# Kernel optimization log

Measured on AMD Instinct MI355X. Metric: run time of the kernel, lower is better.

Reference implementation:

```python
import jax, jax.numpy as jnp
import numpy as np

V, E, H, A, S, B = 32000, 1024, 1024, 10, 512, 64


def setup_inputs() -> dict:
    key = jax.random.key(0)
    ks = jax.random.split(key, 12)
    s = 0.02
    return {
        "dec_input": jax.random.randint(ks[0], (B, 1), 0, V, dtype=jnp.int32),
        "dec_hidden": jax.random.normal(ks[1], (1, B, H), jnp.float32),
        "enc_outputs": jax.random.normal(ks[2], (S, B, H), jnp.float32),
        "emb": jax.random.normal(ks[3], (V, E), jnp.float32) * s,
        "Wa1": jax.random.normal(ks[4], (A, 2 * H), jnp.float32) * s,  # attention layer 1, no bias
        "Wa2": jax.random.normal(ks[5], (1, A), jnp.float32) * s,      # attention layer 2, no bias
        "W_ih": jax.random.normal(ks[6], (3 * H, E + H), jnp.float32) * s,  # GRU input weights (r,z,n)
        "W_hh": jax.random.normal(ks[7], (3 * H, H), jnp.float32) * s,      # GRU hidden weights (r,z,n)
        "b_ih": jnp.zeros((3 * H,), jnp.float32),
        "b_hh": jnp.zeros((3 * H,), jnp.float32),
        "W_out": jax.random.normal(ks[8], (V, H), jnp.float32) * s,
        "b_out": jnp.zeros((V,), jnp.float32),
    }


def reference(dec_input, dec_hidden, enc_outputs, emb, Wa1, Wa2, W_ih, W_hh, b_ih, b_hh, W_out, b_out):
    h_last = dec_hidden[-1]  # [B, H]
    # Bahdanau additive attention over encoder time steps (axis 0)
    hh = jnp.broadcast_to(h_last[None], enc_outputs.shape)        # [S, B, H]
    feats = jnp.concatenate([hh, enc_outputs], axis=-1)           # [S, B, 2H]
    e = jnp.tanh(feats @ Wa1.T) @ Wa2.T                           # [S, B, 1]
    alpha = jax.nn.softmax(e, axis=0)                             # softmax over seq
    c = jnp.sum(alpha * enc_outputs, axis=0)                      # [B, H]
    # embedding lookup for the single decoder step
    x = emb[dec_input[:, 0]]                                      # [B, E]
    xc = jnp.concatenate([x, c], axis=1)                          # [B, E+H]
    # single-step GRU (PyTorch gate order: r, z, n)
    gi = xc @ W_ih.T + b_ih                                       # [B, 3H]
    gh = h_last @ W_hh.T + b_hh                                   # [B, 3H]
    i_r, i_z, i_n = jnp.split(gi, 3, axis=1)
    h_r, h_z, h_n = jnp.split(gh, 3, axis=1)
    r = jax.nn.sigmoid(i_r + h_r)
    z = jax.nn.sigmoid(i_z + h_z)
    n = jnp.tanh(i_n + r * h_n)
    h_new = (1.0 - z) * n + z * h_last                            # [B, H]
    logits = h_new @ W_out.T + b_out                              # [B, V]
    return logits, h_new[None]                                    # ([B,V], [1,B,H])
```

## Files before the change

kernel.cpp:

```cpp
#include <hip/hip_runtime.h>
#include <math.h>

#define Vv 32000
#define Ee 1024
#define Hh 1024
#define Aa 10
#define Ss 512
#define Bb 64
#define Mm (Ss * Bb)

typedef __attribute__((ext_vector_type(8))) short bf16x8;
typedef __attribute__((ext_vector_type(4))) short s16x4;
typedef __attribute__((ext_vector_type(4))) float f32x4;

__device__ inline short f2bf(float f) {
    union { float f; unsigned int u; } v;
    v.f = f;
    unsigned int r = (v.u + 0x7FFFu + ((v.u >> 16) & 1u)) >> 16;
    return (short)r;
}

__device__ inline bf16x8 cvt8(float4 lo, float4 hi) {
    bf16x8 r;
    r[0] = f2bf(lo.x); r[1] = f2bf(lo.y); r[2] = f2bf(lo.z); r[3] = f2bf(lo.w);
    r[4] = f2bf(hi.x); r[5] = f2bf(hi.y); r[6] = f2bf(hi.z); r[7] = f2bf(hi.w);
    return r;
}

__global__ __launch_bounds__(256) void hpart_kernel(const float* __restrict__ Wa1,
                                                    const float* __restrict__ h,
                                                    float* __restrict__ hpart) {
    __shared__ float part[4][16];
    const int b = blockIdx.x, t = threadIdx.x;
    const int w = t >> 6, lane = t & 63;
    const float* hb_ = h + (size_t)b * Hh;
    float p[Aa];
#pragma unroll
    for (int a = 0; a < Aa; a++) p[a] = 0.f;
#pragma unroll
    for (int i = 0; i < 4; i++) {
        const int k = w * 256 + i * 64 + lane;
        const float hv = hb_[k];
#pragma unroll
        for (int a = 0; a < Aa; a++) p[a] += Wa1[a * (2 * Hh) + k] * hv;
    }
#pragma unroll
    for (int a = 0; a < Aa; a++) {
        float v = p[a];
        v += __shfl_xor(v, 1, 64);
        v += __shfl_xor(v, 2, 64);
        v += __shfl_xor(v, 4, 64);
        v += __shfl_xor(v, 8, 64);
        v += __shfl_xor(v, 16, 64);
        v += __shfl_xor(v, 32, 64);
        if (lane == 0) part[w][a] = v;
    }
    __syncthreads();
    if (t < Aa)
        hpart[b * 16 + t] = part[0][t] + part[1][t] + part[2][t] + part[3][t];
}

__global__ __launch_bounds__(256) void scores_e_kernel(
    const float* __restrict__ enc,
    const float* __restrict__ Wa1,
    const float* __restrict__ Wa2,
    const float* __restrict__ hpart,
    float* __restrict__ e_t) {
    const int t = threadIdx.x;
    const int w = t >> 6, lane = t & 63;
    const int col = lane & 15, quad = lane >> 4;
    const int m0 = (blockIdx.x * 4 + w) * 16;
    const int bb = m0 & 63;
    const bool valid = (col < Aa);
    const int wa_row = valid ? col : 0;

    const float* erow = enc + (size_t)(m0 + col) * Hh + quad * 8;
    const float* wrow = Wa1 + (size_t)wa_row * (2 * Hh) + Hh + quad * 8;

    f32x4 acc = {0.f, 0.f, 0.f, 0.f};
#pragma unroll 4
    for (int c = 0; c < 32; c++) {
        float4 a0 = *(const float4*)(erow + c * 32);
        float4 a1 = *(const float4*)(erow + c * 32 + 4);
        bf16x8 af = cvt8(a0, a1);
        bf16x8 bf;
        if (valid) {
            float4 b0 = *(const float4*)(wrow + c * 32);
            float4 b1 = *(const float4*)(wrow + c * 32 + 4);
            bf = cvt8(b0, b1);
        } else {
            bf = (bf16x8){0, 0, 0, 0, 0, 0, 0, 0};
        }
        acc = __builtin_amdgcn_mfma_f32_16x16x32_bf16(af, bf, acc, 0, 0, 0);
    }

    const float w2 = valid ? Wa2[col] : 0.f;
    float v[4];
#pragma unroll
    for (int r = 0; r < 4; r++) {
        const int mr = quad * 4 + r;
        const float hp = valid ? hpart[(bb + mr) * 16 + col] : 0.f;
        v[r] = w2 * tanhf(acc[r] + hp);
    }
#pragma unroll
    for (int r = 0; r < 4; r++) {
        v[r] += __shfl_xor(v[r], 1, 16);
        v[r] += __shfl_xor(v[r], 2, 16);
        v[r] += __shfl_xor(v[r], 4, 16);
        v[r] += __shfl_xor(v[r], 8, 16);
    }
    if (col == 0) {
#pragma unroll
        for (int r = 0; r < 4; r++) {
            const int m = m0 + quad * 4 + r;
            e_t[(size_t)(m & 63) * Ss + (m >> 6)] = v[r];
        }
    }
}

__global__ __launch_bounds__(256) void context_kernel(const float* __restrict__ enc,
                                                      const float* __restrict__ e_t,
                                                      float* __restrict__ cpart) {
    __shared__ float al[Ss];
    __shared__ float sred[8];
    const int b = blockIdx.x, sc = blockIdx.y, t = threadIdx.x;
    const int w = t >> 6, lane = t & 63;

    const float x0 = e_t[(size_t)b * Ss + t];
    const float x1 = e_t[(size_t)b * Ss + 256 + t];
    float mx = fmaxf(x0, x1);
    mx = fmaxf(mx, __shfl_xor(mx, 1, 64));
    mx = fmaxf(mx, __shfl_xor(mx, 2, 64));
    mx = fmaxf(mx, __shfl_xor(mx, 4, 64));
    mx = fmaxf(mx, __shfl_xor(mx, 8, 64));
    mx = fmaxf(mx, __shfl_xor(mx, 16, 64));
    mx = fmaxf(mx, __shfl_xor(mx, 32, 64));
    if (lane == 0) sred[w] = mx;
    __syncthreads();
    const float MX = fmaxf(fmaxf(sred[0], sred[1]), fmaxf(sred[2], sred[3]));
    const float e0 = expf(x0 - MX), e1 = expf(x1 - MX);
    al[t] = e0;
    al[t + 256] = e1;
    float su = e0 + e1;
    su += __shfl_xor(su, 1, 64);
    su += __shfl_xor(su, 2, 64);
    su += __shfl_xor(su, 4, 64);
    su += __shfl_xor(su, 8, 64);
    su += __shfl_xor(su, 16, 64);
    su += __shfl_xor(su, 32, 64);
    if (lane == 0) sred[4 + w] = su;
    __syncthreads();
    const float inv = 1.f / (sred[4] + sred[5] + sred[6] + sred[7]);

    const float4* enc4 = (const float4*)enc;
    float4 acc = {0.f, 0.f, 0.f, 0.f};
    const int s0 = sc * 32;
#pragma unroll 4
    for (int i = 0; i < 32; ++i) {
        const int s = s0 + i;
        const float a = al[s] * inv;
        float4 ev = enc4[(size_t)(s * Bb + b) * 256 + t];
        acc.x += a * ev.x;
        acc.y += a * ev.y;
        acc.z += a * ev.z;
        acc.w += a * ev.w;
    }
    ((float4*)cpart)[((size_t)sc * Bb + b) * 256 + t] = acc;
}

__global__ __launch_bounds__(256) void xc_kernel(const int* __restrict__ dec_input,
                                                 const float* __restrict__ emb,
                                                 const float* __restrict__ cpart,
                                                 const float* __restrict__ h,
                                                 short* __restrict__ xcb,
                                                 short* __restrict__ hb) {
    const int b = blockIdx.x, t = threadIdx.x;
    const int tok = dec_input[b];
    float4 cv = {0.f, 0.f, 0.f, 0.f};
#pragma unroll
    for (int p = 0; p < 16; p++) {
        float4 v = ((const float4*)cpart)[((size_t)p * Bb + b) * 256 + t];
        cv.x += v.x; cv.y += v.y; cv.z += v.z; cv.w += v.w;
    }
    float4 ev = ((const float4*)(emb + (size_t)tok * Ee))[t];
    float4 hv = ((const float4*)(h + (size_t)b * Hh))[t];
    s16x4 e4 = {f2bf(ev.x), f2bf(ev.y), f2bf(ev.z), f2bf(ev.w)};
    s16x4 c4 = {f2bf(cv.x), f2bf(cv.y), f2bf(cv.z), f2bf(cv.w)};
    s16x4 h4v = {f2bf(hv.x), f2bf(hv.y), f2bf(hv.z), f2bf(hv.w)};
    ((s16x4*)(xcb + (size_t)b * 2048))[t] = e4;
    ((s16x4*)(xcb + (size_t)b * 2048 + 1024))[t] = c4;
    ((s16x4*)(hb + (size_t)b * 1024))[t] = h4v;
}

template<int K, int KLEN>
__global__ __launch_bounds__(256) void gemm_mfma_kernel(
    const short* __restrict__ Abf,
    const float* __restrict__ W,
    const float* __restrict__ bias,
    float* __restrict__ C,
    int N) {
    const int t = threadIdx.x;
    const int w = t >> 6, lane = t & 63;
    const int col = lane & 15, quad = lane >> 4;
    const int n0 = blockIdx.x * 64 + w * 16;
    const int kb0 = blockIdx.y * KLEN;

    f32x4 acc[4];
#pragma unroll
    for (int mt = 0; mt < 4; mt++) acc[mt] = (f32x4){0.f, 0.f, 0.f, 0.f};

    const float* wrow = W + (size_t)(n0 + col) * K + kb0 + quad * 8;
    const short* arow = Abf + (size_t)col * K + kb0 + quad * 8;

#pragma unroll 2
    for (int kb = 0; kb < KLEN; kb += 64) {
        float4 w0 = *(const float4*)(wrow + kb);
        float4 w1 = *(const float4*)(wrow + kb + 4);
        float4 w2 = *(const float4*)(wrow + kb + 32);
        float4 w3 = *(const float4*)(wrow + kb + 36);
        bf16x8 bf0 = cvt8(w0, w1);
        bf16x8 bf1 = cvt8(w2, w3);
        bf16x8 a0[4], a1[4];
#pragma unroll
        for (int mt = 0; mt < 4; mt++) {
            a0[mt] = *(const bf16x8*)(arow + (size_t)mt * 16 * K + kb);
            a1[mt] = *(const bf16x8*)(arow + (size_t)mt * 16 * K + kb + 32);
        }
#pragma unroll
        for (int mt = 0; mt < 4; mt++)
            acc[mt] = __builtin_amdgcn_mfma_f32_16x16x32_bf16(a0[mt], bf0, acc[mt], 0, 0, 0);
#pragma unroll
        for (int mt = 0; mt < 4; mt++)
            acc[mt] = __builtin_amdgcn_mfma_f32_16x16x32_bf16(a1[mt], bf1, acc[mt], 0, 0, 0);
    }

    const float bv = (bias != nullptr) ? bias[n0 + col] : 0.f;
    float* Cp = C + (size_t)blockIdx.y * 64 * N;
#pragma unroll
    for (int mt = 0; mt < 4; mt++) {
#pragma unroll
        for (int r = 0; r < 4; r++) {
            int m = mt * 16 + quad * 4 + r;
            Cp[(size_t)m * N + n0 + col] = acc[mt][r] + bv;
        }
    }
}

__global__ __launch_bounds__(256) void gru_kernel(const float* __restrict__ gip,
                                                  const float* __restrict__ ghp,
                                                  const float* __restrict__ b_ih,
                                                  const float* __restrict__ b_hh,
                                                  const float* __restrict__ h,
                                                  float* __restrict__ h_new,
                                                  short* __restrict__ hnb) {
    const int idx = blockIdx.x * 256 + threadIdx.x;
    const int b = idx >> 10, j = idx & 1023;
    const size_t base = (size_t)b * (3 * Hh);
    float ir = b_ih[j], iz = b_ih[Hh + j], in_ = b_ih[2 * Hh + j];
    float hr = b_hh[j], hz = b_hh[Hh + j], hn = b_hh[2 * Hh + j];
#pragma unroll
    for (int p = 0; p < 8; p++) {
        const float* g = gip + (size_t)p * Bb * 3 * Hh + base;
        ir += g[j]; iz += g[Hh + j]; in_ += g[2 * Hh + j];
    }
#pragma unroll
    for (int p = 0; p < 8; p++) {
        const float* g = ghp + (size_t)p * Bb * 3 * Hh + base;
        hr += g[j]; hz += g[Hh + j]; hn += g[2 * Hh + j];
    }
    float r = 1.f / (1.f + expf(-(ir + hr)));
    float z = 1.f / (1.f + expf(-(iz + hz)));
    float n = tanhf(in_ + r * hn);
    float val = (1.f - z) * n + z * h[idx];
    h_new[idx] = val;
    hnb[idx] = f2bf(val);
}

extern "C" void kernel_launch(void* const* d_in, const int* in_sizes, int n_in,
                              void* d_out, int out_size, void* d_ws, size_t ws_size,
                              hipStream_t stream) {
    const int* dec_input = (const int*)d_in[0];
    const float* dec_hidden = (const float*)d_in[1];
    const float* enc = (const float*)d_in[2];
    const float* emb = (const float*)d_in[3];
    const float* Wa1 = (const float*)d_in[4];
    const float* Wa2 = (const float*)d_in[5];
    const float* W_ih = (const float*)d_in[6];
    const float* W_hh = (const float*)d_in[7];
    const float* b_ih = (const float*)d_in[8];
    const float* b_hh = (const float*)d_in[9];
    const float* W_out = (const float*)d_in[10];
    const float* b_out = (const float*)d_in[11];

    float* out = (float*)d_out;
    float* logits = out;
    float* h_new = out + (size_t)Bb * Vv;

    float* ws = (float*)d_ws;
    float* hpart_ptr = ws;
    float* e_ptr = ws + 1024;
    short* xcb_ptr = (short*)(ws + 33792);
    short* hb_ptr = (short*)(ws + 99328);
    short* hnb_ptr = (short*)(ws + 132096);
    float* region1 = ws + 164864;
    float* region2 = ws + 1737728;
    float* cpart_ptr = region1;
    float* gip_ptr = region1;
    float* ghp_ptr = region2;

    hpart_kernel<<<Bb, 256, 0, stream>>>(Wa1, dec_hidden, hpart_ptr);
    scores_e_kernel<<<Mm / 64, 256, 0, stream>>>(enc, Wa1, Wa2, hpart_ptr, e_ptr);
    context_kernel<<<dim3(Bb, 16), 256, 0, stream>>>(enc, e_ptr, cpart_ptr);
    xc_kernel<<<Bb, 256, 0, stream>>>(dec_input, emb, cpart_ptr, dec_hidden,
                                      xcb_ptr, hb_ptr);

    gemm_mfma_kernel<2048, 256><<<dim3(3 * Hh / 64, 8), 256, 0, stream>>>(
        xcb_ptr, W_ih, nullptr, gip_ptr, 3 * Hh);
    gemm_mfma_kernel<1024, 128><<<dim3(3 * Hh / 64, 8), 256, 0, stream>>>(
        hb_ptr, W_hh, nullptr, ghp_ptr, 3 * Hh);

    gru_kernel<<<(Bb * Hh) / 256, 256, 0, stream>>>(gip_ptr, ghp_ptr, b_ih, b_hh,
                                                    dec_hidden, h_new, hnb_ptr);

    gemm_mfma_kernel<1024, 1024><<<dim3(Vv / 64, 1), 256, 0, stream>>>(
        hnb_ptr, W_out, b_out, logits, Vv);
}
```

Before: 447.2 us.

## Fuse all decoder stages into one cooperative persistent kernel with grid syncs

Replaces eight separate kernel launches with a single cooperative kernel of 512 blocks that runs each stage (hpart, scores, softmax-context, xc packing, GRU gemms, GRU cell, output projection) as a phase separated by grid-wide barriers. It also changes the work splits: the context reduction uses 8 sequence chunks instead of 16, and the W_hh gemm uses 2 K-splits instead of 8. The aim is to remove per-launch overhead and inter-kernel gaps. In exchange, phases such as the 500-block output gemm are limited to a fixed grid with 2 blocks per CU, and grid.sync costs are added.

```diff
diff --git a/kernel.cpp b/kernel.cpp
--- a/kernel.cpp
+++ b/kernel.cpp
@@ -1,5 +1,8 @@
 #include <hip/hip_runtime.h>
+#include <hip/hip_cooperative_groups.h>
 #include <math.h>
+
+namespace cg = cooperative_groups;
 
 #define Vv 32000
 #define Ee 1024
@@ -9,6 +12,8 @@
 #define Bb 64
 #define Mm (Ss * Bb)
 
+#define NBLK 512
+
 typedef __attribute__((ext_vector_type(8))) short bf16x8;
 typedef __attribute__((ext_vector_type(4))) short s16x4;
 typedef __attribute__((ext_vector_type(4))) float f32x4;
@@ -27,183 +32,15 @@
     return r;
 }
 
-__global__ __launch_bounds__(256) void hpart_kernel(const float* __restrict__ Wa1,
-                                                    const float* __restrict__ h,
-                                                    float* __restrict__ hpart) {
-    __shared__ float part[4][16];
-    const int b = blockIdx.x, t = threadIdx.x;
-    const int w = t >> 6, lane = t & 63;
-    const float* hb_ = h + (size_t)b * Hh;
-    float p[Aa];
-#pragma unroll
-    for (int a = 0; a < Aa; a++) p[a] = 0.f;
-#pragma unroll
-    for (int i = 0; i < 4; i++) {
-        const int k = w * 256 + i * 64 + lane;
-        const float hv = hb_[k];
-#pragma unroll
-        for (int a = 0; a < Aa; a++) p[a] += Wa1[a * (2 * Hh) + k] * hv;
-    }
-#pragma unroll
-    for (int a = 0; a < Aa; a++) {
-        float v = p[a];
-        v += __shfl_xor(v, 1, 64);
-        v += __shfl_xor(v, 2, 64);
-        v += __shfl_xor(v, 4, 64);
-        v += __shfl_xor(v, 8, 64);
-        v += __shfl_xor(v, 16, 64);
-        v += __shfl_xor(v, 32, 64);
-        if (lane == 0) part[w][a] = v;
-    }
-    __syncthreads();
-    if (t < Aa)
-        hpart[b * 16 + t] = part[0][t] + part[1][t] + part[2][t] + part[3][t];
-}
-
-__global__ __launch_bounds__(256) void scores_e_kernel(
-    const float* __restrict__ enc,
-    const float* __restrict__ Wa1,
-    const float* __restrict__ Wa2,
-    const float* __restrict__ hpart,
-    float* __restrict__ e_t) {
-    const int t = threadIdx.x;
-    const int w = t >> 6, lane = t & 63;
+template<int K, int KLEN>
+__device__ __forceinline__ void gemm_phase(const short* __restrict__ Abf,
+                                           const float* __restrict__ W,
+                                           const float* __restrict__ bias,
+                                           float* __restrict__ C, int N,
+                                           int nb, int kp, int w, int lane) {
     const int col = lane & 15, quad = lane >> 4;
-    const int m0 = (blockIdx.x * 4 + w) * 16;
-    const int bb = m0 & 63;
-    const bool valid = (col < Aa);
-    const int wa_row = valid ? col : 0;
-
-    const float* erow = enc + (size_t)(m0 + col) * Hh + quad * 8;
-    const float* wrow = Wa1 + (size_t)wa_row * (2 * Hh) + Hh + quad * 8;
-
-    f32x4 acc = {0.f, 0.f, 0.f, 0.f};
-#pragma unroll 4
-    for (int c = 0; c < 32; c++) {
-        float4 a0 = *(const float4*)(erow + c * 32);
-        float4 a1 = *(const float4*)(erow + c * 32 + 4);
-        bf16x8 af = cvt8(a0, a1);
-        bf16x8 bf;
-        if (valid) {
-            float4 b0 = *(const float4*)(wrow + c * 32);
-            float4 b1 = *(const float4*)(wrow + c * 32 + 4);
-            bf = cvt8(b0, b1);
-        } else {
-            bf = (bf16x8){0, 0, 0, 0, 0, 0, 0, 0};
-        }
-        acc = __builtin_amdgcn_mfma_f32_16x16x32_bf16(af, bf, acc, 0, 0, 0);
-    }
-
-    const float w2 = valid ? Wa2[col] : 0.f;
-    float v[4];
-#pragma unroll
-    for (int r = 0; r < 4; r++) {
-        const int mr = quad * 4 + r;
-        const float hp = valid ? hpart[(bb + mr) * 16 + col] : 0.f;
-        v[r] = w2 * tanhf(acc[r] + hp);
-    }
-#pragma unroll
-    for (int r = 0; r < 4; r++) {
-        v[r] += __shfl_xor(v[r], 1, 16);
-        v[r] += __shfl_xor(v[r], 2, 16);
-        v[r] += __shfl_xor(v[r], 4, 16);
-        v[r] += __shfl_xor(v[r], 8, 16);
-    }
-    if (col == 0) {
-#pragma unroll
-        for (int r = 0; r < 4; r++) {
-            const int m = m0 + quad * 4 + r;
-            e_t[(size_t)(m & 63) * Ss + (m >> 6)] = v[r];
-        }
-    }
-}
-
-__global__ __launch_bounds__(256) void context_kernel(const float* __restrict__ enc,
-                                                      const float* __restrict__ e_t,
-                                                      float* __restrict__ cpart) {
-    __shared__ float al[Ss];
-    __shared__ float sred[8];
-    const int b = blockIdx.x, sc = blockIdx.y, t = threadIdx.x;
-    const int w = t >> 6, lane = t & 63;
-
-    const float x0 = e_t[(size_t)b * Ss + t];
-    const float x1 = e_t[(size_t)b * Ss + 256 + t];
-    float mx = fmaxf(x0, x1);
-    mx = fmaxf(mx, __shfl_xor(mx, 1, 64));
-    mx = fmaxf(mx, __shfl_xor(mx, 2, 64));
-    mx = fmaxf(mx, __shfl_xor(mx, 4, 64));
-    mx = fmaxf(mx, __shfl_xor(mx, 8, 64));
-    mx = fmaxf(mx, __shfl_xor(mx, 16, 64));
-    mx = fmaxf(mx, __shfl_xor(mx, 32, 64));
-    if (lane == 0) sred[w] = mx;
-    __syncthreads();
-    const float MX = fmaxf(fmaxf(sred[0], sred[1]), fmaxf(sred[2], sred[3]));
-    const float e0 = expf(x0 - MX), e1 = expf(x1 - MX);
-    al[t] = e0;
-    al[t + 256] = e1;
-    float su = e0 + e1;
-    su += __shfl_xor(su, 1, 64);
-    su += __shfl_xor(su, 2, 64);
-    su += __shfl_xor(su, 4, 64);
-    su += __shfl_xor(su, 8, 64);
-    su += __shfl_xor(su, 16, 64);
-    su += __shfl_xor(su, 32, 64);
-    if (lane == 0) sred[4 + w] = su;
-    __syncthreads();
-    const float inv = 1.f / (sred[4] + sred[5] + sred[6] + sred[7]);
-
-    const float4* enc4 = (const float4*)enc;
-    float4 acc = {0.f, 0.f, 0.f, 0.f};
-    const int s0 = sc * 32;
-#pragma unroll 4
-    for (int i = 0; i < 32; ++i) {
-        const int s = s0 + i;
-        const float a = al[s] * inv;
-        float4 ev = enc4[(size_t)(s * Bb + b) * 256 + t];
-        acc.x += a * ev.x;
-        acc.y += a * ev.y;
-        acc.z += a * ev.z;
-        acc.w += a * ev.w;
-    }
-    ((float4*)cpart)[((size_t)sc * Bb + b) * 256 + t] = acc;
-}
-
-__global__ __launch_bounds__(256) void xc_kernel(const int* __restrict__ dec_input,
-                                                 const float* __restrict__ emb,
-                                                 const float* __restrict__ cpart,
-                                                 const float* __restrict__ h,
-                                                 short* __restrict__ xcb,
-                                                 short* __restrict__ hb) {
-    const int b = blockIdx.x, t = threadIdx.x;
-    const int tok = dec_input[b];
-    float4 cv = {0.f, 0.f, 0.f, 0.f};
-#pragma unroll
-    for (int p = 0; p < 16; p++) {
-        float4 v = ((const float4*)cpart)[((size_t)p * Bb + b) * 256 + t];
-        cv.x += v.x; cv.y += v.y; cv.z += v.z; cv.w += v.w;
-    }
-    float4 ev = ((const float4*)(emb + (size_t)tok * Ee))[t];
-    float4 hv = ((const float4*)(h + (size_t)b * Hh))[t];
-    s16x4 e4 = {f2bf(ev.x), f2bf(ev.y), f2bf(ev.z), f2bf(ev.w)};
-    s16x4 c4 = {f2bf(cv.x), f2bf(cv.y), f2bf(cv.z), f2bf(cv.w)};
-    s16x4 h4v = {f2bf(hv.x), f2bf(hv.y), f2bf(hv.z), f2bf(hv.w)};
-    ((s16x4*)(xcb + (size_t)b * 2048))[t] = e4;
-    ((s16x4*)(xcb + (size_t)b * 2048 + 1024))[t] = c4;
-    ((s16x4*)(hb + (size_t)b * 1024))[t] = h4v;
-}
-
-template<int K, int KLEN>
-__global__ __launch_bounds__(256) void gemm_mfma_kernel(
-    const short* __restrict__ Abf,
-    const float* __restrict__ W,
-    const float* __restrict__ bias,
-    float* __restrict__ C,
-    int N) {
-    const int t = threadIdx.x;
-    const int w = t >> 6, lane = t & 63;
-    const int col = lane & 15, quad = lane >> 4;
-    const int n0 = blockIdx.x * 64 + w * 16;
-    const int kb0 = blockIdx.y * KLEN;
+    const int n0 = nb * 64 + w * 16;
+    const int kb0 = kp * KLEN;
 
     f32x4 acc[4];
 #pragma unroll
@@ -235,7 +72,7 @@
     }
 
     const float bv = (bias != nullptr) ? bias[n0 + col] : 0.f;
-    float* Cp = C + (size_t)blockIdx.y * 64 * N;
+    float* Cp = C + (size_t)kp * 64 * N;
 #pragma unroll
     for (int mt = 0; mt < 4; mt++) {
 #pragma unroll
@@ -246,34 +83,223 @@
     }
 }
 
-__global__ __launch_bounds__(256) void gru_kernel(const float* __restrict__ gip,
-                                                  const float* __restrict__ ghp,
-                                                  const float* __restrict__ b_ih,
-                                                  const float* __restrict__ b_hh,
-                                                  const float* __restrict__ h,
-                                                  float* __restrict__ h_new,
-                                                  short* __restrict__ hnb) {
-    const int idx = blockIdx.x * 256 + threadIdx.x;
-    const int b = idx >> 10, j = idx & 1023;
-    const size_t base = (size_t)b * (3 * Hh);
-    float ir = b_ih[j], iz = b_ih[Hh + j], in_ = b_ih[2 * Hh + j];
-    float hr = b_hh[j], hz = b_hh[Hh + j], hn = b_hh[2 * Hh + j];
-#pragma unroll
-    for (int p = 0; p < 8; p++) {
-        const float* g = gip + (size_t)p * Bb * 3 * Hh + base;
-        ir += g[j]; iz += g[Hh + j]; in_ += g[2 * Hh + j];
-    }
-#pragma unroll
-    for (int p = 0; p < 8; p++) {
-        const float* g = ghp + (size_t)p * Bb * 3 * Hh + base;
-        hr += g[j]; hz += g[Hh + j]; hn += g[2 * Hh + j];
-    }
-    float r = 1.f / (1.f + expf(-(ir + hr)));
-    float z = 1.f / (1.f + expf(-(iz + hz)));
-    float n = tanhf(in_ + r * hn);
-    float val = (1.f - z) * n + z * h[idx];
-    h_new[idx] = val;
-    hnb[idx] = f2bf(val);
+__global__ __launch_bounds__(256, 2) void mega_kernel(
+    const int* __restrict__ dec_input,
+    const float* __restrict__ dec_hidden,
+    const float* __restrict__ enc,
+    const float* __restrict__ emb,
+    const float* __restrict__ Wa1,
+    const float* __restrict__ Wa2,
+    const float* __restrict__ W_ih,
+    const float* __restrict__ W_hh,
+    const float* __restrict__ b_ih,
+    const float* __restrict__ b_hh,
+    const float* __restrict__ W_out,
+    const float* __restrict__ b_out,
+    float* __restrict__ ws,
+    float* __restrict__ logits,
+    float* __restrict__ h_new) {
+    cg::grid_group grid = cg::this_grid();
+    const int blk = blockIdx.x;
+    const int t = threadIdx.x;
+    const int w = t >> 6, lane = t & 63;
+
+    float* hpart = ws;
+    float* e_t   = ws + 1024;
+    short* xcb   = (short*)(ws + 33792);
+    short* hb    = (short*)(ws + 99328);
+    short* hnb   = (short*)(ws + 132096);
+    float* cpart = ws + 164864;
+    float* gip   = ws + 689152;
+    float* ghp   = ws + 2262016;
+
+    __shared__ float sm[Ss];
+    __shared__ float sred[8];
+    __shared__ float part4[4][16];
+
+    if (blk < Bb) {
+        const int b = blk;
+        const float* hb_ = dec_hidden + (size_t)b * Hh;
+        float p[Aa];
+#pragma unroll
+        for (int a = 0; a < Aa; a++) p[a] = 0.f;
+#pragma unroll
+        for (int i = 0; i < 4; i++) {
+            const int k = w * 256 + i * 64 + lane;
+            const float hv = hb_[k];
+#pragma unroll
+            for (int a = 0; a < Aa; a++) p[a] += Wa1[a * (2 * Hh) + k] * hv;
+        }
+#pragma unroll
+        for (int a = 0; a < Aa; a++) {
+            float v = p[a];
+            v += __shfl_xor(v, 1, 64);
+            v += __shfl_xor(v, 2, 64);
+            v += __shfl_xor(v, 4, 64);
+            v += __shfl_xor(v, 8, 64);
+            v += __shfl_xor(v, 16, 64);
+            v += __shfl_xor(v, 32, 64);
+            if (lane == 0) part4[w][a] = v;
+        }
+        __syncthreads();
+        if (t < Aa)
+            hpart[b * 16 + t] = part4[0][t] + part4[1][t] + part4[2][t] + part4[3][t];
+    }
+    grid.sync();
+
+    {
+        const int col = lane & 15, quad = lane >> 4;
+        const int m0 = (blk * 4 + w) * 16;
+        const int bb = m0 & 63;
+        const bool valid = (col < Aa);
+        const int wa_row = valid ? col : 0;
+
+        const float* erow = enc + (size_t)(m0 + col) * Hh + quad * 8;
+        const float* wrow = Wa1 + (size_t)wa_row * (2 * Hh) + Hh + quad * 8;
+
+        f32x4 acc = {0.f, 0.f, 0.f, 0.f};
+#pragma unroll 4
+        for (int c = 0; c < 32; c++) {
+            float4 a0 = *(const float4*)(erow + c * 32);
+            float4 a1 = *(const float4*)(erow + c * 32 + 4);
+            bf16x8 af = cvt8(a0, a1);
+            bf16x8 bf;
+            if (valid) {
+                float4 b0 = *(const float4*)(wrow + c * 32);
+                float4 b1 = *(const float4*)(wrow + c * 32 + 4);
+                bf = cvt8(b0, b1);
+            } else {
+                bf = (bf16x8){0, 0, 0, 0, 0, 0, 0, 0};
+            }
+            acc = __builtin_amdgcn_mfma_f32_16x16x32_bf16(af, bf, acc, 0, 0, 0);
+        }
+
+        const float w2 = valid ? Wa2[col] : 0.f;
+        float v[4];
+#pragma unroll
+        for (int r = 0; r < 4; r++) {
+            const int mr = quad * 4 + r;
+            const float hp = valid ? hpart[(bb + mr) * 16 + col] : 0.f;
+            v[r] = w2 * tanhf(acc[r] + hp);
+        }
+#pragma unroll
+        for (int r = 0; r < 4; r++) {
+            v[r] += __shfl_xor(v[r], 1, 16);
+            v[r] += __shfl_xor(v[r], 2, 16);
+            v[r] += __shfl_xor(v[r], 4, 16);
+            v[r] += __shfl_xor(v[r], 8, 16);
+        }
+        if (col == 0) {
+#pragma unroll
+            for (int r = 0; r < 4; r++) {
+                const int m = m0 + quad * 4 + r;
+                e_t[(size_t)(m & 63) * Ss + (m >> 6)] = v[r];
+            }
+        }
+    }
+    grid.sync();
+
+    {
+        const int b = blk & 63, sc = blk >> 6;
+        const float x0 = e_t[(size_t)b * Ss + t];
+        const float x1 = e_t[(size_t)b * Ss + 256 + t];
+        float mx = fmaxf(x0, x1);
+        mx = fmaxf(mx, __shfl_xor(mx, 1, 64));
+        mx = fmaxf(mx, __shfl_xor(mx, 2, 64));
+        mx = fmaxf(mx, __shfl_xor(mx, 4, 64));
+        mx = fmaxf(mx, __shfl_xor(mx, 8, 64));
+        mx = fmaxf(mx, __shfl_xor(mx, 16, 64));
+        mx = fmaxf(mx, __shfl_xor(mx, 32, 64));
+        if (lane == 0) sred[w] = mx;
+        __syncthreads();
+        const float MX = fmaxf(fmaxf(sred[0], sred[1]), fmaxf(sred[2], sred[3]));
+        const float e0 = expf(x0 - MX), e1 = expf(x1 - MX);
+        sm[t] = e0;
+        sm[t + 256] = e1;
+        float su = e0 + e1;
+        su += __shfl_xor(su, 1, 64);
+        su += __shfl_xor(su, 2, 64);
+        su += __shfl_xor(su, 4, 64);
+        su += __shfl_xor(su, 8, 64);
+        su += __shfl_xor(su, 16, 64);
+        su += __shfl_xor(su, 32, 64);
+        if (lane == 0) sred[4 + w] = su;
+        __syncthreads();
+        const float inv = 1.f / (sred[4] + sred[5] + sred[6] + sred[7]);
+
+        const float4* enc4 = (const float4*)enc;
+        float4 acc = {0.f, 0.f, 0.f, 0.f};
+        const int s0 = sc * 64;
+#pragma unroll 4
+        for (int i = 0; i < 64; ++i) {
+            const int s = s0 + i;
+            const float a = sm[s] * inv;
+            float4 ev = enc4[(size_t)(s * Bb + b) * 256 + t];
+            acc.x += a * ev.x;
+            acc.y += a * ev.y;
+            acc.z += a * ev.z;
+            acc.w += a * ev.w;
+        }
+        ((float4*)cpart)[((size_t)sc * Bb + b) * 256 + t] = acc;
+    }
+    grid.sync();
+
+    if (blk < Bb) {
+        const int b = blk;
+        const int tok = dec_input[b];
+        float4 cv = {0.f, 0.f, 0.f, 0.f};
+#pragma unroll
+        for (int p = 0; p < 8; p++) {
+            float4 v = ((const float4*)cpart)[((size_t)p * Bb + b) * 256 + t];
+            cv.x += v.x; cv.y += v.y; cv.z += v.z; cv.w += v.w;
+        }
+        float4 ev = ((const float4*)(emb + (size_t)tok * Ee))[t];
+        float4 hv = ((const float4*)(dec_hidden + (size_t)b * Hh))[t];
+        s16x4 e4 = {f2bf(ev.x), f2bf(ev.y), f2bf(ev.z), f2bf(ev.w)};
+        s16x4 c4 = {f2bf(cv.x), f2bf(cv.y), f2bf(cv.z), f2bf(cv.w)};
+        s16x4 h4v = {f2bf(hv.x), f2bf(hv.y), f2bf(hv.z), f2bf(hv.w)};
+        ((s16x4*)(xcb + (size_t)b * 2048))[t] = e4;
+        ((s16x4*)(xcb + (size_t)b * 2048 + 1024))[t] = c4;
+        ((s16x4*)(hb + (size_t)b * 1024))[t] = h4v;
+    }
+    grid.sync();
+
+    if (blk < 384) {
+        gemm_phase<2048, 256>(xcb, W_ih, nullptr, gip, 3 * Hh, blk % 48, blk / 48, w, lane);
+    } else if (blk < 480) {
+        const int t2 = blk - 384;
+        gemm_phase<1024, 512>(hb, W_hh, nullptr, ghp, 3 * Hh, t2 % 48, t2 / 48, w, lane);
+    }
+    grid.sync();
+
+    if (t < 128) {
+        const int idx = blk * 128 + t;
+        const int b = idx >> 10, j = idx & 1023;
+        const size_t base = (size_t)b * (3 * Hh);
+        float ir = b_ih[j], iz = b_ih[Hh + j], in_ = b_ih[2 * Hh + j];
+        float hr = b_hh[j], hz = b_hh[Hh + j], hn = b_hh[2 * Hh + j];
+#pragma unroll
+        for (int p = 0; p < 8; p++) {
+            const float* g = gip + (size_t)p * Bb * 3 * Hh + base;
+            ir += g[j]; iz += g[Hh + j]; in_ += g[2 * Hh + j];
+        }
+#pragma unroll
+        for (int p = 0; p < 2; p++) {
+            const float* g = ghp + (size_t)p * Bb * 3 * Hh + base;
+            hr += g[j]; hz += g[Hh + j]; hn += g[2 * Hh + j];
+        }
+        float r = 1.f / (1.f + expf(-(ir + hr)));
+        float z = 1.f / (1.f + expf(-(iz + hz)));
+        float n = tanhf(in_ + r * hn);
+        float val = (1.f - z) * n + z * dec_hidden[idx];
+        h_new[idx] = val;
+        hnb[idx] = f2bf(val);
+    }
+    grid.sync();
+
+    if (blk < Vv / 64) {
+        gemm_phase<1024, 1024>(hnb, W_out, b_out, logits, Vv, blk, 0, w, lane);
+    }
 }
 
 extern "C" void kernel_launch(void* const* d_in, const int* in_sizes, int n_in,
@@ -295,33 +321,14 @@
     float* out = (float*)d_out;
     float* logits = out;
     float* h_new = out + (size_t)Bb * Vv;
-
     float* ws = (float*)d_ws;
-    float* hpart_ptr = ws;
-    float* e_ptr = ws + 1024;
-    short* xcb_ptr = (short*)(ws + 33792);
-    short* hb_ptr = (short*)(ws + 99328);
-    short* hnb_ptr = (short*)(ws + 132096);
-    float* region1 = ws + 164864;
-    float* region2 = ws + 1737728;
-    float* cpart_ptr = region1;
-    float* gip_ptr = region1;
-    float* ghp_ptr = region2;
-
-    hpart_kernel<<<Bb, 256, 0, stream>>>(Wa1, dec_hidden, hpart_ptr);
-    scores_e_kernel<<<Mm / 64, 256, 0, stream>>>(enc, Wa1, Wa2, hpart_ptr, e_ptr);
-    context_kernel<<<dim3(Bb, 16), 256, 0, stream>>>(enc, e_ptr, cpart_ptr);
-    xc_kernel<<<Bb, 256, 0, stream>>>(dec_input, emb, cpart_ptr, dec_hidden,
-                                      xcb_ptr, hb_ptr);
-
-    gemm_mfma_kernel<2048, 256><<<dim3(3 * Hh / 64, 8), 256, 0, stream>>>(
-        xcb_ptr, W_ih, nullptr, gip_ptr, 3 * Hh);
-    gemm_mfma_kernel<1024, 128><<<dim3(3 * Hh / 64, 8), 256, 0, stream>>>(
-        hb_ptr, W_hh, nullptr, ghp_ptr, 3 * Hh);
-
-    gru_kernel<<<(Bb * Hh) / 256, 256, 0, stream>>>(gip_ptr, ghp_ptr, b_ih, b_hh,
-                                                    dec_hidden, h_new, hnb_ptr);
-
-    gemm_mfma_kernel<1024, 1024><<<dim3(Vv / 64, 1), 256, 0, stream>>>(
-        hnb_ptr, W_out, b_out, logits, Vv);
-}
+
+    void* args[] = {
+        (void*)&dec_input, (void*)&dec_hidden, (void*)&enc, (void*)&emb,
+        (void*)&Wa1, (void*)&Wa2, (void*)&W_ih, (void*)&W_hh,
+        (void*)&b_ih, (void*)&b_hh, (void*)&W_out, (void*)&b_out,
+        (void*)&ws, (void*)&logits, (void*)&h_new
+    };
+    hipLaunchCooperativeKernel((void*)mega_kernel, dim3(NBLK), dim3(256),
+                               args, 0, stream);
+}
```

New measurement: 796.2 us. 78.0% more time.
